# Performance work log

Hardware: AMD Instinct MI355X
Metric: run time of the kernel (lower is better)

Reference implementation:

```python
import jax, jax.numpy as jnp
import numpy as np

B, S, H = 32, 1024, 512  # batch, src_len, hidden_dim


def setup_inputs() -> dict:
    key = jax.random.key(0)
    k1, k2, k3, k4, k5 = jax.random.split(key, 5)
    hidden = jax.random.normal(k1, (B, H), dtype=jnp.float32)
    encoder_outputs = jax.random.normal(k2, (B, S, 2 * H), dtype=jnp.float32)
    # nn.Linear(3H, H): weight stored here as [3H, H] (input-major) with bias [H]
    W = jax.random.normal(k3, (3 * H, H), dtype=jnp.float32) / np.sqrt(3 * H)
    b = jax.random.normal(k4, (H,), dtype=jnp.float32) * 0.01
    v = jax.random.normal(k5, (H,), dtype=jnp.float32) / np.sqrt(H)
    return {"hidden": hidden, "encoder_outputs": encoder_outputs, "W": W, "b": b, "v": v}


def reference(hidden, encoder_outputs, W, b, v):
    # concat((repeat(hidden), encoder_outputs)) @ W  ==  hidden @ W[:H] (broadcast) + enc @ W[H:]
    Wh, We = W[:H], W[H:]                         # [H,H], [2H,H]
    h_proj = hidden @ Wh                           # [B,H]
    e_proj = jnp.einsum('bse,eh->bsh', encoder_outputs, We)  # [B,S,H]
    energy = jnp.tanh(h_proj[:, None, :] + e_proj + b)       # [B,S,H]
    # bmm(v[B,1,H], energy^T[B,H,S]) -> scores [B,S]
    scores = jnp.einsum('bsh,h->bs', energy, v)
    return jax.nn.softmax(scores, axis=1)
```

## Files before the change

kernel.cpp:

```cpp
#include <hip/hip_runtime.h>
#include <math.h>

#define B_ 32
#define S_ 1024
#define H_ 512
#define K_ 1024
#define M_ (B_ * S_)

typedef __attribute__((ext_vector_type(8))) short bf16x8;
typedef __attribute__((ext_vector_type(16))) float f32x16;

__device__ __forceinline__ void split_bf16(float f, unsigned short& hi, unsigned short& lo) {
    unsigned u = __float_as_uint(f);
    unsigned r = u + 0x8000u;
    hi = (unsigned short)(r >> 16);
    float fh = __uint_as_float(r & 0xffff0000u);
    float res = f - fh;
    lo = (unsigned short)((__float_as_uint(res) + 0x8000u) >> 16);
}

__device__ __forceinline__ void split8_store(const float4& x, const float4& y,
                                             unsigned short* hiP, unsigned short* loP) {
    float f[8] = {x.x, x.y, x.z, x.w, y.x, y.y, y.z, y.w};
    unsigned hr[8], lr[8];
    #pragma unroll
    for (int i = 0; i < 8; ++i) {
        unsigned u = __float_as_uint(f[i]);
        unsigned r = u + 0x8000u;
        hr[i] = r;
        float fh = __uint_as_float(r & 0xffff0000u);
        lr[i] = __float_as_uint(f[i] - fh) + 0x8000u;
    }
    uint4 Hv, Lv;
    Hv.x = __builtin_amdgcn_perm(hr[1], hr[0], 0x07060302u);
    Hv.y = __builtin_amdgcn_perm(hr[3], hr[2], 0x07060302u);
    Hv.z = __builtin_amdgcn_perm(hr[5], hr[4], 0x07060302u);
    Hv.w = __builtin_amdgcn_perm(hr[7], hr[6], 0x07060302u);
    Lv.x = __builtin_amdgcn_perm(lr[1], lr[0], 0x07060302u);
    Lv.y = __builtin_amdgcn_perm(lr[3], lr[2], 0x07060302u);
    Lv.z = __builtin_amdgcn_perm(lr[5], lr[4], 0x07060302u);
    Lv.w = __builtin_amdgcn_perm(lr[7], lr[6], 0x07060302u);
    *reinterpret_cast<uint4*>(hiP) = Hv;
    *reinterpret_cast<uint4*>(loP) = Lv;
}

__device__ __forceinline__ float fast_tanh(float x) {
    float xc = fminf(fmaxf(x, -15.f), 15.f);
    float t = __expf(2.0f * xc);
    return (t - 1.0f) * __builtin_amdgcn_rcpf(t + 1.0f);
}

__device__ __forceinline__ void async_copy16(const void* g, void* l) {
    __builtin_amdgcn_global_load_lds(
        (const __attribute__((address_space(1))) void*)g,
        (__attribute__((address_space(3))) void*)l, 16, 0, 0);
}

__global__ __launch_bounds__(256) void prep_kernel(
    const float* __restrict__ hidden, const float* __restrict__ W,
    const float* __restrict__ bias, float* __restrict__ hb,
    unsigned short* __restrict__ Wh, unsigned short* __restrict__ Wl)
{
    __shared__ float red[4][64];
    __shared__ float t[32][33];
    const int bx = blockIdx.x;
    if (bx < 256) {
        const int tid = threadIdx.x;
        const int h0  = (bx & 7) * 64;
        const int b   = bx >> 3;
        const int h   = h0 + (tid & 63);
        const int ks  = tid >> 6;
        const float* hrow = hidden + b * H_;
        float acc = 0.f;
        #pragma unroll 8
        for (int k = ks * 128; k < ks * 128 + 128; ++k)
            acc = fmaf(hrow[k], W[(size_t)k * H_ + h], acc);
        red[ks][tid & 63] = acc;
        __syncthreads();
        if (tid < 64)
            hb[b * H_ + h0 + tid] = red[0][tid] + red[1][tid] + red[2][tid]
                                  + red[3][tid] + bias[h0 + tid];
    } else {
        const float* We = W + (size_t)H_ * H_;
        const int cx = bx - 256;
        const int k0 = (cx & 31) * 32, n0 = (cx >> 5) * 32;
        const int tx = threadIdx.x & 31, ty = threadIdx.x >> 5;
        #pragma unroll
        for (int j = 0; j < 4; ++j) {
            const int k = ty + 8 * j;
            t[k][tx] = We[(size_t)(k0 + k) * H_ + n0 + tx];
        }
        __syncthreads();
        #pragma unroll
        for (int j = 0; j < 4; ++j) {
            const int n    = ty + 8 * j;
            const int ncol = n0 + n;
            const int k    = k0 + tx;
            unsigned short hi, lo;
            split_bf16(t[tx][n], hi, lo);
            const int c     = ncol >> 5;
            const int tt    = k >> 4;
            const int lane_ = ((k >> 3) & 1) * 32 + (ncol & 31);
            const size_t s  = ((size_t)(c * 64 + tt) * 64 + lane_) * 8 + (k & 7);
            Wh[s] = hi;
            Wl[s] = lo;
        }
    }
}

__global__ __launch_bounds__(512, 2) void gemm_fused(
    const float* __restrict__ EO,
    const unsigned short* __restrict__ Bth,
    const unsigned short* __restrict__ Btl,
    const float* __restrict__ hb, const float* __restrict__ v,
    float* __restrict__ partial)
{
    __shared__ unsigned short ldsA[2][2][8192];
    __shared__ unsigned short ldsB[2][2][8192];

    const int tid  = threadIdx.x;
    const int bid  = blockIdx.x;
    const int jb   = bid >> 3;
    const int mt   = (bid & 7) * 16 + (jb >> 1);
    const int nt   = jb & 1;
    const int row0 = mt * 256;
    const int col0 = nt * 256;
    const int batch = row0 >> 10;

    const int lane   = tid & 63;
    const int wave   = tid >> 6;
    const int wm     = wave >> 2, wn = wave & 3;
    const int lane32 = lane & 31, kh = lane >> 5;

    size_t gA[2];
    int offAw[2];
    #pragma unroll
    for (int s = 0; s < 2; ++s) {
        const int seg = tid + 512 * s;
        const int m = seg >> 2, sg = seg & 3;
        gA[s]    = (size_t)(row0 + m) * K_ + sg * 8;
        offAw[s] = ((m >> 5) * 2 + (sg >> 1)) * 512
                 + ((sg & 1) * 32 + ((m & 31) ^ sg)) * 8;
    }
    const unsigned short* gBh = Bth + ((size_t)(nt * 8 + wave) * 32768 + lane * 8);
    const unsigned short* gBl = Btl + ((size_t)(nt * 8 + wave) * 32768 + lane * 8);
    const int offBw = wave * 1024;

    f32x16 acc[4][2];
    #pragma unroll
    for (int fi = 0; fi < 4; ++fi)
        #pragma unroll
        for (int fj = 0; fj < 2; ++fj)
            #pragma unroll
            for (int e = 0; e < 16; ++e)
                acc[fi][fj][e] = 0.f;

    float4 a0[2], a1[2];
    #pragma unroll
    for (int s = 0; s < 2; ++s) {
        a0[s] = *reinterpret_cast<const float4*>(EO + gA[s]);
        a1[s] = *reinterpret_cast<const float4*>(EO + gA[s] + 4);
    }
    #pragma unroll
    for (int ks = 0; ks < 2; ++ks) {
        async_copy16(gBh + ks * 512, &ldsB[0][0][offBw + ks * 512]);
        async_copy16(gBl + ks * 512, &ldsB[0][1][offBw + ks * 512]);
    }
    #pragma unroll
    for (int s = 0; s < 2; ++s)
        split8_store(a0[s], a1[s], &ldsA[0][0][offAw[s]], &ldsA[0][1][offAw[s]]);

    for (int i = 0; i < 32; ++i) {
        __syncthreads();
        const int cur = i & 1, nxt = cur ^ 1;
        if (i < 31) {
            const int k0n = 32 * (i + 1);
            #pragma unroll
            for (int s = 0; s < 2; ++s) {
                a0[s] = *reinterpret_cast<const float4*>(EO + gA[s] + k0n);
                a1[s] = *reinterpret_cast<const float4*>(EO + gA[s] + k0n + 4);
            }
            const int tnxt = 2 * (i + 1);
            #pragma unroll
            for (int ks = 0; ks < 2; ++ks) {
                async_copy16(gBh + (tnxt + ks) * 512, &ldsB[nxt][0][offBw + ks * 512]);
                async_copy16(gBl + (tnxt + ks) * 512, &ldsB[nxt][1][offBw + ks * 512]);
            }
        }

        bf16x8 b_h[2][2], b_l[2][2];
        #pragma unroll
        for (int fj = 0; fj < 2; ++fj)
            #pragma unroll
            for (int ks = 0; ks < 2; ++ks) {
                const int baseB = ((wn * 2 + fj) * 2 + ks) * 512 + lane * 8;
                b_h[fj][ks] = *reinterpret_cast<const bf16x8*>(&ldsB[cur][0][baseB]);
                b_l[fj][ks] = *reinterpret_cast<const bf16x8*>(&ldsB[cur][1][baseB]);
            }
        #pragma unroll
        for (int fi = 0; fi < 4; ++fi) {
            bf16x8 a_h[2], a_l[2];
            #pragma unroll
            for (int ks = 0; ks < 2; ++ks) {
                const int baseA = ((wm * 4 + fi) * 2 + ks) * 512
                                + (kh * 32 + (lane32 ^ (2 * ks + kh))) * 8;
                a_h[ks] = *reinterpret_cast<const bf16x8*>(&ldsA[cur][0][baseA]);
                a_l[ks] = *reinterpret_cast<const bf16x8*>(&ldsA[cur][1][baseA]);
            }
            #pragma unroll
            for (int fj = 0; fj < 2; ++fj)
                #pragma unroll
                for (int ks = 0; ks < 2; ++ks) {
                    acc[fi][fj] = __builtin_amdgcn_mfma_f32_32x32x16_bf16(
                        a_h[ks], b_h[fj][ks], acc[fi][fj], 0, 0, 0);
                    acc[fi][fj] = __builtin_amdgcn_mfma_f32_32x32x16_bf16(
                        a_h[ks], b_l[fj][ks], acc[fi][fj], 0, 0, 0);
                    acc[fi][fj] = __builtin_amdgcn_mfma_f32_32x32x16_bf16(
                        a_l[ks], b_h[fj][ks], acc[fi][fj], 0, 0, 0);
                }
        }

        if (i < 31) {
            #pragma unroll
            for (int s = 0; s < 2; ++s)
                split8_store(a0[s], a1[s],
                             &ldsA[nxt][0][offAw[s]], &ldsA[nxt][1][offAw[s]]);
        }
    }

    const float* hb_row = hb + batch * H_;
    float hbv[2], vv[2];
    #pragma unroll
    for (int fj = 0; fj < 2; ++fj) {
        const int c = col0 + (wn * 2 + fj) * 32 + lane32;
        hbv[fj] = hb_row[c];
        vv[fj]  = v[c];
    }
    float* red = reinterpret_cast<float*>(&ldsA[0][0][0]);
    #pragma unroll
    for (int fi = 0; fi < 4; ++fi)
        #pragma unroll
        for (int r = 0; r < 16; ++r) {
            float rs = 0.f;
            #pragma unroll
            for (int fj = 0; fj < 2; ++fj)
                rs = fmaf(fast_tanh(acc[fi][fj][r] + hbv[fj]), vv[fj], rs);
            rs += __shfl_xor(rs, 1, 64);
            rs += __shfl_xor(rs, 2, 64);
            rs += __shfl_xor(rs, 4, 64);
            rs += __shfl_xor(rs, 8, 64);
            rs += __shfl_xor(rs, 16, 64);
            if (lane32 == 0) {
                const int row = wm * 128 + fi * 32 + (r & 3) + 8 * (r >> 2) + 4 * kh;
                red[row * 4 + wn] = rs;
            }
        }
    __syncthreads();
    if (tid < 256)
        partial[(size_t)nt * M_ + row0 + tid] =
            red[tid * 4] + red[tid * 4 + 1] + red[tid * 4 + 2] + red[tid * 4 + 3];
}

__global__ __launch_bounds__(256) void softmax_kernel(
    const float* __restrict__ partial, float* __restrict__ out)
{
    const int b = blockIdx.x;
    const int tid = threadIdx.x;
    float val[4];
    float lmax = -3.0e38f;
    #pragma unroll
    for (int q = 0; q < 4; ++q) {
        const int idx = b * S_ + tid + 256 * q;
        float sum = partial[idx] + partial[M_ + idx];
        val[q] = sum;
        lmax = fmaxf(lmax, sum);
    }
    #pragma unroll
    for (int off = 32; off > 0; off >>= 1)
        lmax = fmaxf(lmax, __shfl_down(lmax, off, 64));
    __shared__ float wmax[4];
    if ((tid & 63) == 0) wmax[tid >> 6] = lmax;
    __syncthreads();
    const float gmax = fmaxf(fmaxf(wmax[0], wmax[1]), fmaxf(wmax[2], wmax[3]));
    float lsum = 0.0f;
    #pragma unroll
    for (int q = 0; q < 4; ++q) {
        val[q] = expf(val[q] - gmax);
        lsum += val[q];
    }
    #pragma unroll
    for (int off = 32; off > 0; off >>= 1)
        lsum += __shfl_down(lsum, off, 64);
    __shared__ float wsum[4];
    if ((tid & 63) == 0) wsum[tid >> 6] = lsum;
    __syncthreads();
    const float inv = 1.0f / (wsum[0] + wsum[1] + wsum[2] + wsum[3]);
    #pragma unroll
    for (int q = 0; q < 4; ++q)
        out[b * S_ + tid + 256 * q] = val[q] * inv;
}

extern "C" void kernel_launch(void* const* d_in, const int* in_sizes, int n_in,
                              void* d_out, int out_size, void* d_ws, size_t ws_size,
                              hipStream_t stream) {
    const float* hidden = (const float*)d_in[0];
    const float* EO     = (const float*)d_in[1];
    const float* W      = (const float*)d_in[2];
    const float* bias   = (const float*)d_in[3];
    const float* v      = (const float*)d_in[4];
    float* out          = (float*)d_out;

    float* hb      = (float*)d_ws;
    float* partial = hb + B_ * H_;
    unsigned short* Wth = (unsigned short*)(partial + 4 * M_);
    unsigned short* Wtl = Wth + (size_t)H_ * K_;

    prep_kernel<<<768, 256, 0, stream>>>(hidden, W, bias, hb, Wth, Wtl);
    gemm_fused<<<dim3(256), 512, 0, stream>>>(EO, Wth, Wtl, hb, v, partial);
    softmax_kernel<<<B_, 256, 0, stream>>>(partial, out);
}
```

Before: 287.7 us.

## Triple-buffer B tiles with counted vmcnt waits and raised MFMA priority

B operand tiles move from a double LDS buffer to a three-deep ring, so the async copies are issued two iterations ahead. The __syncthreads at the top of the loop is replaced by an explicit s_waitcnt vmcnt(4) plus barrier at the end, which leaves the newest copies in flight. The MFMA section is also wrapped in s_setprio. LDS use grows by 32KB per block, which could reduce occupancy under launch_bounds(512,2), and the hand-written waitcnt counts must exactly match the number of outstanding loads.

```diff
diff --git a/kernel.cpp b/kernel.cpp
--- a/kernel.cpp
+++ b/kernel.cpp
@@ -116,7 +116,7 @@
     float* __restrict__ partial)
 {
     __shared__ unsigned short ldsA[2][2][8192];
-    __shared__ unsigned short ldsB[2][2][8192];
+    __shared__ unsigned short ldsB[3][2][8192];
 
     const int tid  = threadIdx.x;
     const int bid  = blockIdx.x;
@@ -162,40 +162,51 @@
         a1[s] = *reinterpret_cast<const float4*>(EO + gA[s] + 4);
     }
     #pragma unroll
-    for (int ks = 0; ks < 2; ++ks) {
-        async_copy16(gBh + ks * 512, &ldsB[0][0][offBw + ks * 512]);
-        async_copy16(gBl + ks * 512, &ldsB[0][1][offBw + ks * 512]);
-    }
-    #pragma unroll
     for (int s = 0; s < 2; ++s)
         split8_store(a0[s], a1[s], &ldsA[0][0][offAw[s]], &ldsA[0][1][offAw[s]]);
-
-    for (int i = 0; i < 32; ++i) {
-        __syncthreads();
-        const int cur = i & 1, nxt = cur ^ 1;
-        if (i < 31) {
-            const int k0n = 32 * (i + 1);
+    #pragma unroll
+    for (int ks = 0; ks < 2; ++ks) {
+        async_copy16(gBh + (0 + ks) * 512, &ldsB[0][0][offBw + ks * 512]);
+        async_copy16(gBl + (0 + ks) * 512, &ldsB[0][1][offBw + ks * 512]);
+    }
+    #pragma unroll
+    for (int ks = 0; ks < 2; ++ks) {
+        async_copy16(gBh + (2 + ks) * 512, &ldsB[1][0][offBw + ks * 512]);
+        async_copy16(gBl + (2 + ks) * 512, &ldsB[1][1][offBw + ks * 512]);
+    }
+    asm volatile("s_waitcnt vmcnt(4) lgkmcnt(0)\n\ts_barrier" ::: "memory");
+
+    int bc = 0;
+    for (int j = 0; j < 32; ++j) {
+        const int cur = j & 1, nxt = cur ^ 1;
+        const int bn  = (bc >= 1) ? bc - 1 : 2;
+
+        if (j < 31) {
+            const int k0n = 32 * (j + 1);
             #pragma unroll
             for (int s = 0; s < 2; ++s) {
                 a0[s] = *reinterpret_cast<const float4*>(EO + gA[s] + k0n);
                 a1[s] = *reinterpret_cast<const float4*>(EO + gA[s] + k0n + 4);
             }
-            const int tnxt = 2 * (i + 1);
+        }
+        if (j < 30) {
+            const int tnxt = 2 * (j + 2);
             #pragma unroll
             for (int ks = 0; ks < 2; ++ks) {
-                async_copy16(gBh + (tnxt + ks) * 512, &ldsB[nxt][0][offBw + ks * 512]);
-                async_copy16(gBl + (tnxt + ks) * 512, &ldsB[nxt][1][offBw + ks * 512]);
-            }
-        }
-
+                async_copy16(gBh + (tnxt + ks) * 512, &ldsB[bn][0][offBw + ks * 512]);
+                async_copy16(gBl + (tnxt + ks) * 512, &ldsB[bn][1][offBw + ks * 512]);
+            }
+        }
+
+        __builtin_amdgcn_s_setprio(1);
         bf16x8 b_h[2][2], b_l[2][2];
         #pragma unroll
         for (int fj = 0; fj < 2; ++fj)
             #pragma unroll
             for (int ks = 0; ks < 2; ++ks) {
                 const int baseB = ((wn * 2 + fj) * 2 + ks) * 512 + lane * 8;
-                b_h[fj][ks] = *reinterpret_cast<const bf16x8*>(&ldsB[cur][0][baseB]);
-                b_l[fj][ks] = *reinterpret_cast<const bf16x8*>(&ldsB[cur][1][baseB]);
+                b_h[fj][ks] = *reinterpret_cast<const bf16x8*>(&ldsB[bc][0][baseB]);
+                b_l[fj][ks] = *reinterpret_cast<const bf16x8*>(&ldsB[bc][1][baseB]);
             }
         #pragma unroll
         for (int fi = 0; fi < 4; ++fi) {
@@ -219,13 +230,22 @@
                         a_l[ks], b_h[fj][ks], acc[fi][fj], 0, 0, 0);
                 }
         }
-
-        if (i < 31) {
+        __builtin_amdgcn_s_setprio(0);
+
+        if (j < 30) {
             #pragma unroll
             for (int s = 0; s < 2; ++s)
                 split8_store(a0[s], a1[s],
                              &ldsA[nxt][0][offAw[s]], &ldsA[nxt][1][offAw[s]]);
-        }
+            asm volatile("s_waitcnt vmcnt(4) lgkmcnt(0)\n\ts_barrier" ::: "memory");
+        } else if (j == 30) {
+            #pragma unroll
+            for (int s = 0; s < 2; ++s)
+                split8_store(a0[s], a1[s],
+                             &ldsA[nxt][0][offAw[s]], &ldsA[nxt][1][offAw[s]]);
+            asm volatile("s_waitcnt vmcnt(0) lgkmcnt(0)\n\ts_barrier" ::: "memory");
+        }
+        bc = (bc == 2) ? 0 : bc + 1;
     }
 
     const float* hb_row = hb + batch * H_;
```

Measured after the change: 287.1 us. No clear change (-0.2%).

## Deepen GEMM pipeline with triple-buffered B and two-phase ping-pong MFMA schedule

Applied to the files above, without the earlier changes.

Adds a third LDS buffer for the B (weight) tiles so B is prefetched two k-steps ahead, and holds two register sets for the A (fp32 activation) loads so global reads run a step further ahead. Each k-step is split into two MFMA phases, each fed by its own half of the A fragments. The phases are separated by explicit s_barrier, waitcnt, sched_barrier and setprio calls, so that LDS writes and global loads interleave with MFMA work across waves. This is meant to hide memory latency behind the 3-pass split-bf16 MFMAs. In exchange it adds more barriers per step, more LDS (which may lower occupancy at 2 blocks per CU), and hand-tuned vmcnt counts that can stall or become wrong if the compiler reorders memory ops.

```diff
diff --git a/kernel.cpp b/kernel.cpp
--- a/kernel.cpp
+++ b/kernel.cpp
@@ -116,7 +116,7 @@
     float* __restrict__ partial)
 {
     __shared__ unsigned short ldsA[2][2][8192];
-    __shared__ unsigned short ldsB[2][2][8192];
+    __shared__ unsigned short ldsB[3][2][8192];
 
     const int tid  = threadIdx.x;
     const int bid  = blockIdx.x;
@@ -155,78 +155,124 @@
             for (int e = 0; e < 16; ++e)
                 acc[fi][fj][e] = 0.f;
 
-    float4 a0[2], a1[2];
+    float4 a0A[2], a1A[2], a0B[2], a1B[2];
     #pragma unroll
     for (int s = 0; s < 2; ++s) {
-        a0[s] = *reinterpret_cast<const float4*>(EO + gA[s]);
-        a1[s] = *reinterpret_cast<const float4*>(EO + gA[s] + 4);
+        a0A[s] = *reinterpret_cast<const float4*>(EO + gA[s]);
+        a1A[s] = *reinterpret_cast<const float4*>(EO + gA[s] + 4);
     }
     #pragma unroll
     for (int ks = 0; ks < 2; ++ks) {
-        async_copy16(gBh + ks * 512, &ldsB[0][0][offBw + ks * 512]);
-        async_copy16(gBl + ks * 512, &ldsB[0][1][offBw + ks * 512]);
+        async_copy16(gBh + (0 + ks) * 512, &ldsB[0][0][offBw + ks * 512]);
+        async_copy16(gBl + (0 + ks) * 512, &ldsB[0][1][offBw + ks * 512]);
+    }
+    #pragma unroll
+    for (int ks = 0; ks < 2; ++ks) {
+        async_copy16(gBh + (2 + ks) * 512, &ldsB[1][0][offBw + ks * 512]);
+        async_copy16(gBl + (2 + ks) * 512, &ldsB[1][1][offBw + ks * 512]);
     }
     #pragma unroll
     for (int s = 0; s < 2; ++s)
-        split8_store(a0[s], a1[s], &ldsA[0][0][offAw[s]], &ldsA[0][1][offAw[s]]);
-
-    for (int i = 0; i < 32; ++i) {
-        __syncthreads();
-        const int cur = i & 1, nxt = cur ^ 1;
-        if (i < 31) {
-            const int k0n = 32 * (i + 1);
-            #pragma unroll
-            for (int s = 0; s < 2; ++s) {
-                a0[s] = *reinterpret_cast<const float4*>(EO + gA[s] + k0n);
-                a1[s] = *reinterpret_cast<const float4*>(EO + gA[s] + k0n + 4);
-            }
-            const int tnxt = 2 * (i + 1);
-            #pragma unroll
-            for (int ks = 0; ks < 2; ++ks) {
-                async_copy16(gBh + (tnxt + ks) * 512, &ldsB[nxt][0][offBw + ks * 512]);
-                async_copy16(gBl + (tnxt + ks) * 512, &ldsB[nxt][1][offBw + ks * 512]);
-            }
-        }
-
-        bf16x8 b_h[2][2], b_l[2][2];
-        #pragma unroll
-        for (int fj = 0; fj < 2; ++fj)
-            #pragma unroll
-            for (int ks = 0; ks < 2; ++ks) {
-                const int baseB = ((wn * 2 + fj) * 2 + ks) * 512 + lane * 8;
-                b_h[fj][ks] = *reinterpret_cast<const bf16x8*>(&ldsB[cur][0][baseB]);
-                b_l[fj][ks] = *reinterpret_cast<const bf16x8*>(&ldsB[cur][1][baseB]);
-            }
-        #pragma unroll
-        for (int fi = 0; fi < 4; ++fi) {
-            bf16x8 a_h[2], a_l[2];
-            #pragma unroll
-            for (int ks = 0; ks < 2; ++ks) {
-                const int baseA = ((wm * 4 + fi) * 2 + ks) * 512
-                                + (kh * 32 + (lane32 ^ (2 * ks + kh))) * 8;
-                a_h[ks] = *reinterpret_cast<const bf16x8*>(&ldsA[cur][0][baseA]);
-                a_l[ks] = *reinterpret_cast<const bf16x8*>(&ldsA[cur][1][baseA]);
-            }
-            #pragma unroll
-            for (int fj = 0; fj < 2; ++fj)
-                #pragma unroll
-                for (int ks = 0; ks < 2; ++ks) {
-                    acc[fi][fj] = __builtin_amdgcn_mfma_f32_32x32x16_bf16(
-                        a_h[ks], b_h[fj][ks], acc[fi][fj], 0, 0, 0);
-                    acc[fi][fj] = __builtin_amdgcn_mfma_f32_32x32x16_bf16(
-                        a_h[ks], b_l[fj][ks], acc[fi][fj], 0, 0, 0);
-                    acc[fi][fj] = __builtin_amdgcn_mfma_f32_32x32x16_bf16(
-                        a_l[ks], b_h[fj][ks], acc[fi][fj], 0, 0, 0);
-                }
-        }
-
-        if (i < 31) {
-            #pragma unroll
-            for (int s = 0; s < 2; ++s)
-                split8_store(a0[s], a1[s],
-                             &ldsA[nxt][0][offAw[s]], &ldsA[nxt][1][offAw[s]]);
-        }
-    }
+        split8_store(a0A[s], a1A[s], &ldsA[0][0][offAw[s]], &ldsA[0][1][offAw[s]]);
+    #pragma unroll
+    for (int s = 0; s < 2; ++s) {
+        a0B[s] = *reinterpret_cast<const float4*>(EO + gA[s] + 32);
+        a1B[s] = *reinterpret_cast<const float4*>(EO + gA[s] + 32 + 4);
+    }
+    asm volatile("s_waitcnt vmcnt(8) lgkmcnt(0)" ::: "memory");
+    __builtin_amdgcn_s_barrier();
+
+#define PHASE_MFMA(fb)                                                         \
+    _Pragma("unroll") for (int ks = 0; ks < 2; ++ks)                           \
+      _Pragma("unroll") for (int p = 0; p < 3; ++p)                            \
+        _Pragma("unroll") for (int f2 = 0; f2 < 2; ++f2)                       \
+          _Pragma("unroll") for (int fj = 0; fj < 2; ++fj) {                   \
+            acc[(fb) + f2][fj] = __builtin_amdgcn_mfma_f32_32x32x16_bf16(      \
+                (p == 2) ? a_l[f2][ks] : a_h[f2][ks],                          \
+                (p == 1) ? b_l[fj][ks] : b_h[fj][ks],                          \
+                acc[(fb) + f2][fj], 0, 0, 0);                                  \
+          }
+
+#define K_STEP(J, CUR, S0, S1, I0, I1)                                         \
+  {                                                                            \
+    const int nxt = (CUR) ^ 1;                                                 \
+    const int bn  = (bc >= 1) ? bc - 1 : 2;                     \
+           \
+    bf16x8 b_h[2][2], b_l[2][2];                                               \
+    _Pragma("unroll") for (int fj = 0; fj < 2; ++fj)                           \
+      _Pragma("unroll") for (int ks = 0; ks < 2; ++ks) {                       \
+        const int baseB = ((wn * 2 + fj) * 2 + ks) * 512 + lane * 8;           \
+        b_h[fj][ks] = *reinterpret_cast<const bf16x8*>(&ldsB[bc][0][baseB]);   \
+        b_l[fj][ks] = *reinterpret_cast<const bf16x8*>(&ldsB[bc][1][baseB]);   \
+      }                                                                        \
+    {                                                                          \
+      bf16x8 a_h[2][2], a_l[2][2];                                             \
+      _Pragma("unroll") for (int f2 = 0; f2 < 2; ++f2)                         \
+        _Pragma("unroll") for (int ks = 0; ks < 2; ++ks) {                     \
+          const int baseA = ((wm * 4 + f2) * 2 + ks) * 512                     \
+                          + (kh * 32 + (lane32 ^ (2 * ks + kh))) * 8;          \
+          a_h[f2][ks] = *reinterpret_cast<const bf16x8*>(&ldsA[CUR][0][baseA]);\
+          a_l[f2][ks] = *reinterpret_cast<const bf16x8*>(&ldsA[CUR][1][baseA]);\
+        }                                                                      \
+      __builtin_amdgcn_s_barrier();                                            \
+      asm volatile("s_waitcnt lgkmcnt(0)" ::: "memory");                       \
+      __builtin_amdgcn_sched_barrier(0);                                       \
+      __builtin_amdgcn_s_setprio(1);                                           \
+      PHASE_MFMA(0)                                                            \
+      __builtin_amdgcn_s_setprio(0);                                           \
+      __builtin_amdgcn_s_barrier();                                            \
+    }                                                                          \
+       \
+    {                                                                          \
+      bf16x8 a_h[2][2], a_l[2][2];                                             \
+      _Pragma("unroll") for (int f2 = 0; f2 < 2; ++f2)                         \
+        _Pragma("unroll") for (int ks = 0; ks < 2; ++ks) {                     \
+          const int baseA = ((wm * 4 + 2 + f2) * 2 + ks) * 512                 \
+                          + (kh * 32 + (lane32 ^ (2 * ks + kh))) * 8;          \
+          a_h[f2][ks] = *reinterpret_cast<const bf16x8*>(&ldsA[CUR][0][baseA]);\
+          a_l[f2][ks] = *reinterpret_cast<const bf16x8*>(&ldsA[CUR][1][baseA]);\
+        }                                                                      \
+      if ((J) < 30) {                              \
+        const int tnxt = 2 * ((J) + 2);                                        \
+        _Pragma("unroll") for (int ks = 0; ks < 2; ++ks) {                     \
+          async_copy16(gBh + (tnxt + ks) * 512, &ldsB[bn][0][offBw + ks*512]); \
+          async_copy16(gBl + (tnxt + ks) * 512, &ldsB[bn][1][offBw + ks*512]); \
+        }                                                                      \
+      }                                                                        \
+      if ((J) < 31) {          \
+        _Pragma("unroll") for (int s = 0; s < 2; ++s)                          \
+          split8_store(S0[s], S1[s],                                           \
+                       &ldsA[nxt][0][offAw[s]], &ldsA[nxt][1][offAw[s]]);      \
+      }                                                                        \
+      if ((J) < 30) {                                        \
+        const int k0n = 32 * ((J) + 2);                                        \
+        _Pragma("unroll") for (int s = 0; s < 2; ++s) {                        \
+          I0[s] = *reinterpret_cast<const float4*>(EO + gA[s] + k0n);          \
+          I1[s] = *reinterpret_cast<const float4*>(EO + gA[s] + k0n + 4);      \
+        }                                                                      \
+      }                                                                        \
+      __builtin_amdgcn_s_barrier();                                            \
+      asm volatile("s_waitcnt lgkmcnt(0)" ::: "memory");                       \
+      __builtin_amdgcn_sched_barrier(0);                                       \
+      __builtin_amdgcn_s_setprio(1);                                           \
+      PHASE_MFMA(2)                                                            \
+      __builtin_amdgcn_s_setprio(0);                                           \
+      if ((J) < 30) { asm volatile("s_waitcnt vmcnt(8)" ::: "memory"); }       \
+      else          { asm volatile("s_waitcnt vmcnt(0)" ::: "memory"); }       \
+      __builtin_amdgcn_s_barrier();                                            \
+    }                                                                          \
+    bc = (bc == 2) ? 0 : bc + 1;                                               \
+  }
+
+    int bc = 0;
+    #pragma unroll 1
+    for (int jj = 0; jj < 16; ++jj) {
+        const int je = 2 * jj;
+        K_STEP(je,     0, a0B, a1B, a0A, a1A)
+        K_STEP(je + 1, 1, a0A, a1A, a0B, a1B)
+    }
+#undef K_STEP
+#undef PHASE_MFMA
 
     const float* hb_row = hb + batch * H_;
     float hbv[2], vv[2];
```

New measurement: 285.0 us. About the same (-1.0%).
